# Kernel tuning notes

Measured on AMD Instinct MI355X. Metric: run time of the kernel, lower is better.

## Reference

```python
import jax, jax.numpy as jnp
import numpy as np

B, N, D, H = 2, 2048, 1024, 16
DH = D // H  # 64


def setup_inputs() -> dict:
    key = jax.random.key(0)
    k1, k2, k3, k4, k5 = jax.random.split(key, 5)
    x = jax.random.normal(k1, (B, N, D), dtype=jnp.float32)
    # per-head kqv Linear weights, stacked: [H, D, 3*DH] (acts as x @ W)
    W_kqv = jax.random.normal(k2, (H, D, 3 * DH), dtype=jnp.float32) * 0.02
    b_kqv = jax.random.normal(k3, (H, 3 * DH), dtype=jnp.float32) * 0.02
    W_proj = jax.random.normal(k4, (D, D), dtype=jnp.float32) * 0.02
    b_proj = jax.random.normal(k5, (D,), dtype=jnp.float32) * 0.02
    return {"x": x, "W_kqv": W_kqv, "b_kqv": b_kqv, "W_proj": W_proj, "b_proj": b_proj}


def reference(x, W_kqv, b_kqv, W_proj, b_proj):
    # per-head projections, all heads batched: [B, H, N, 3*DH]
    kqv = jnp.einsum('bnd,hde->bhne', x, W_kqv) + b_kqv[None, :, None, :]
    # original chunk order is k, q, v
    k, q, v = jnp.split(kqv, 3, axis=-1)  # each [B, H, N, DH]
    # scores: A = q @ k^T / sqrt(DH)  -> [B, H, N, N]
    A = jnp.einsum('bhnd,bhmd->bhnm', q, k) / jnp.sqrt(jnp.asarray(DH, x.dtype))
    causal = jnp.tril(jnp.ones((N, N), dtype=bool))
    A = jnp.where(causal[None, None, :, :], A, -jnp.inf)
    attn = jax.nn.softmax(A, axis=-1)
    sa = jnp.einsum('bhnm,bhmd->bhnd', attn, v)          # [B, H, N, DH]
    sa = sa.transpose(0, 2, 1, 3).reshape(B, N, D)        # concat heads
    out = sa @ W_proj.T + b_proj                          # output projection
    return out
```

## Files before the change

kernel.cpp:

```cpp
#include <hip/hip_runtime.h>
#include <hip/hip_bf16.h>
#include <cstdint>
#include <cstddef>

#define B_  2
#define N_  2048
#define D_  1024
#define H_  16
#define DH_ 64
#define E3_ 192

typedef __attribute__((ext_vector_type(8))) short short8;
typedef __attribute__((ext_vector_type(8))) unsigned short ushort8v;
typedef __attribute__((ext_vector_type(4))) float floatx4;

static __device__ __forceinline__ unsigned short f2bf(float f) {
  union { float f; unsigned u; } c; c.f = f;
  unsigned r = c.u + 0x7fffu + ((c.u >> 16) & 1u);
  return (unsigned short)(r >> 16);
}

#define MFMA(a,b,c) __builtin_amdgcn_mfma_f32_16x16x32_bf16((a),(b),(c),0,0,0)

#define GL_LDS16(g, l) __builtin_amdgcn_global_load_lds( \
    (const __attribute__((address_space(1))) void*)(g),  \
    (__attribute__((address_space(3))) void*)(l), 16, 0, 0)

__global__ __launch_bounds__(256) void k_prep(const float* __restrict__ x,
                                              const float* __restrict__ Wkqv,
                                              const float* __restrict__ Wproj,
                                              unsigned short* __restrict__ Xb,
                                              unsigned short* __restrict__ Wt,
                                              unsigned short* __restrict__ Wpb) {
  __shared__ float tile[64][65];
  int bx = blockIdx.x, t = threadIdx.x;
  if (bx < 2048 || bx >= 2816) {
    const float* in = (bx < 2048) ? x : Wproj;
    unsigned short* out = (bx < 2048) ? Xb : Wpb;
    int i = ((bx < 2048) ? bx : bx - 2816) * 256 + t;
    const float4* p = (const float4*)in + (size_t)i * 2;
    float4 a = p[0], b = p[1];
    ushort8v o;
    o[0]=f2bf(a.x); o[1]=f2bf(a.y); o[2]=f2bf(a.z); o[3]=f2bf(a.w);
    o[4]=f2bf(b.x); o[5]=f2bf(b.y); o[6]=f2bf(b.z); o[7]=f2bf(b.w);
    *((ushort8v*)out + i) = o;
    return;
  }
  int idx = bx - 2048;
  int d0 = (idx & 15) * 64, rem = idx >> 4;
  int cat = rem % 3, h = rem / 3, e0 = cat * 64;
  const float* Wp = Wkqv + (size_t)h * D_ * E3_;
  int dr = t >> 2, ec = (t & 3) * 16;
#pragma unroll
  for (int j = 0; j < 16; j += 4) {
    float4 wv = *(const float4*)&Wp[(size_t)(d0 + dr) * E3_ + e0 + ec + j];
    tile[dr][ec + j + 0] = wv.x; tile[dr][ec + j + 1] = wv.y;
    tile[dr][ec + j + 2] = wv.z; tile[dr][ec + j + 3] = wv.w;
  }
  __syncthreads();
  int er = t >> 2, dc = (t & 3) * 16;
  ushort8v o0, o1;
#pragma unroll
  for (int j = 0; j < 8; j++) o0[j] = f2bf(tile[dc + j][er]);
#pragma unroll
  for (int j = 0; j < 8; j++) o1[j] = f2bf(tile[dc + 8 + j][er]);
  size_t o = ((size_t)(cat * 1024 + h * 64 + er)) * D_ + d0 + dc;
  *(ushort8v*)&Wt[o]     = o0;
  *(ushort8v*)&Wt[o + 8] = o1;
}

__global__ __launch_bounds__(256) void k_qkv(const unsigned short* __restrict__ Xb,
                                             const unsigned short* __restrict__ Wt,
                                             const float* __restrict__ bkqv,
                                             unsigned short* __restrict__ Qb,
                                             unsigned short* __restrict__ Kb,
                                             unsigned short* __restrict__ Vt) {
  __shared__ unsigned short Alds[2][128 * 32];
  __shared__ unsigned short Blds[2][128 * 32];
  int t = threadIdx.x;
  int m0 = blockIdx.x * 128, c0 = blockIdx.y * 128;
  int wave = t >> 6, lane = t & 63, quad = lane >> 4, l16 = lane & 15;
  int wm = (wave >> 1) * 64, wn = (wave & 1) * 64;
  floatx4 acc[4][4];
#pragma unroll
  for (int i = 0; i < 4; i++)
#pragma unroll
    for (int j = 0; j < 4; j++) acc[i][j] = (floatx4){0.f, 0.f, 0.f, 0.f};

  const unsigned short* gA = Xb + (size_t)(m0 + wave * 32 + (lane >> 2)) * D_ + (lane & 3) * 8;
  const unsigned short* gB = Wt + (size_t)(c0 + wave * 32 + (lane >> 2)) * D_ + (lane & 3) * 8;
  int lofs = (wave * 32) * 32;

  GL_LDS16(gA,            &Alds[0][lofs]);
  GL_LDS16(gA + 16 * D_,  &Alds[0][lofs + 16 * 32]);
  GL_LDS16(gB,            &Blds[0][lofs]);
  GL_LDS16(gB + 16 * D_,  &Blds[0][lofs + 16 * 32]);

  for (int i = 0; i < 32; i++) {
    int buf = i & 1;
    __syncthreads();
    if (i + 1 < 32) {
      int k0 = (i + 1) * 32;
      GL_LDS16(gA + k0,            &Alds[buf ^ 1][lofs]);
      GL_LDS16(gA + k0 + 16 * D_,  &Alds[buf ^ 1][lofs + 16 * 32]);
      GL_LDS16(gB + k0,            &Blds[buf ^ 1][lofs]);
      GL_LDS16(gB + k0 + 16 * D_,  &Blds[buf ^ 1][lofs + 16 * 32]);
    }
    short8 a[4], b[4];
#pragma unroll
    for (int mi = 0; mi < 4; mi++) a[mi] = *(const short8*)&Alds[buf][(wm + mi * 16 + l16) * 32 + quad * 8];
#pragma unroll
    for (int ni = 0; ni < 4; ni++) b[ni] = *(const short8*)&Blds[buf][(wn + ni * 16 + l16) * 32 + quad * 8];
#pragma unroll
    for (int mi = 0; mi < 4; mi++)
#pragma unroll
      for (int ni = 0; ni < 4; ni++) acc[mi][ni] = MFMA(a[mi], b[ni], acc[mi][ni]);
  }

  int cat = c0 >> 10;
#pragma unroll
  for (int mi = 0; mi < 4; mi++)
#pragma unroll
    for (int ni = 0; ni < 4; ni++) {
      int colp = c0 + wn + ni * 16 + l16;
      int h = (colp >> 6) & 15;
      int e = colp & 63;
      int grow = m0 + wm + mi * 16 + quad * 4;
      int b = grow >> 11, n0 = grow & (N_ - 1);
      int bh = b * H_ + h;
      float bias = bkqv[h * E3_ + cat * 64 + e];
      floatx4 v = acc[mi][ni];
      if (cat == 0) {
        size_t base = ((size_t)bh * N_ + n0) * DH_ + e;
#pragma unroll
        for (int r = 0; r < 4; r++) Kb[base + (size_t)r * DH_] = f2bf(v[r] + bias);
      } else if (cat == 1) {
        size_t base = ((size_t)bh * N_ + n0) * DH_ + e;
#pragma unroll
        for (int r = 0; r < 4; r++) Qb[base + (size_t)r * DH_] = f2bf((v[r] + bias) * 0.125f);
      } else {
        ushort4 pk;
        pk.x = f2bf(v[0] + bias); pk.y = f2bf(v[1] + bias);
        pk.z = f2bf(v[2] + bias); pk.w = f2bf(v[3] + bias);
        *(ushort4*)&Vt[((size_t)bh * DH_ + e) * N_ + n0] = pk;
      }
    }
}

#define PSTR 72
__global__ __launch_bounds__(256) void k_flash(const unsigned short* __restrict__ Qb,
                                               const unsigned short* __restrict__ Kb,
                                               const unsigned short* __restrict__ Vt,
                                               unsigned short* __restrict__ sab) {
  int bh = blockIdx.x;
  int yr = blockIdx.y, g = yr >> 3, o = yr & 7;
  int qb = (g == 0) ? o : (g == 1) ? 31 - o : (g == 2) ? 8 + o : 23 - o;
  int q0b = qb * 64;
  int wave = threadIdx.x >> 6;
  int lane = threadIdx.x & 63, quad = lane >> 4, l16 = lane & 15;
  const unsigned short* Qp = Qb + (size_t)bh * N_ * DH_;
  const unsigned short* Kp = Kb + (size_t)bh * N_ * DH_;
  const unsigned short* Vp = Vt + (size_t)bh * DH_ * N_;
  __shared__ unsigned short Klds[2][2 * 64 * 32];
  __shared__ unsigned short Vlds[2][2 * 64 * 32];
  __shared__ unsigned short Plds[4][16 * PSTR];
  unsigned short* P = Plds[wave];

  int q0w = q0b + wave * 16;
  short8 qf0 = *(const short8*)&Qp[(q0w + l16) * DH_ + quad * 8];
  short8 qf1 = *(const short8*)&Qp[(q0w + l16) * DH_ + 32 + quad * 8];

  const unsigned short* gK = Kp + (size_t)(wave * 16 + (lane >> 2)) * DH_ + (lane & 3) * 8;
  const unsigned short* gV = Vp + (size_t)(wave * 16 + (lane >> 2)) * N_ + (lane & 3) * 8;
  int lofs = (wave * 16) * 32;

  floatx4 O[4];
  float lr[4];
#pragma unroll
  for (int r = 0; r < 4; r++) { O[r] = (floatx4){0.f, 0.f, 0.f, 0.f}; lr[r] = 0.f; }

  int nt = (q0b >> 6) + 1;
  GL_LDS16(gK,      &Klds[0][lofs]);
  GL_LDS16(gK + 32, &Klds[0][lofs + 64 * 32]);
  GL_LDS16(gV,      &Vlds[0][lofs]);
  GL_LDS16(gV + 32, &Vlds[0][lofs + 64 * 32]);

  for (int i = 0; i < nt; i++) {
    int buf = i & 1;
    __syncthreads();
    if (i + 1 < nt) {
      int kvn = (i + 1) << 6;
      GL_LDS16(gK + (size_t)kvn * DH_,      &Klds[buf ^ 1][lofs]);
      GL_LDS16(gK + (size_t)kvn * DH_ + 32, &Klds[buf ^ 1][lofs + 64 * 32]);
      GL_LDS16(gV + kvn,                    &Vlds[buf ^ 1][lofs]);
      GL_LDS16(gV + kvn + 32,               &Vlds[buf ^ 1][lofs + 64 * 32]);
    }
    short8 kf[4][2], vf[4][2];
#pragma unroll
    for (int c = 0; c < 4; c++) {
      kf[c][0] = *(const short8*)&Klds[buf][(c * 16 + l16) * 32 + quad * 8];
      kf[c][1] = *(const short8*)&Klds[buf][(64 + c * 16 + l16) * 32 + quad * 8];
      vf[c][0] = *(const short8*)&Vlds[buf][(c * 16 + l16) * 32 + quad * 8];
      vf[c][1] = *(const short8*)&Vlds[buf][(64 + c * 16 + l16) * 32 + quad * 8];
    }
    floatx4 s[4];
#pragma unroll
    for (int c = 0; c < 4; c++) {
      s[c] = (floatx4){0.f, 0.f, 0.f, 0.f};
      s[c] = MFMA(qf0, kf[c][0], s[c]);
      s[c] = MFMA(qf1, kf[c][1], s[c]);
    }
    if (i == nt - 1) {
#pragma unroll
      for (int c = 0; c < 4; c++)
#pragma unroll
        for (int r = 0; r < 4; r++) {
          int row = wave * 16 + quad * 4 + r;
          if (c * 16 + l16 > row) s[c][r] = -1e30f;
        }
    }
#pragma unroll
    for (int c = 0; c < 4; c++)
#pragma unroll
      for (int r = 0; r < 4; r++)
        s[c][r] = __builtin_amdgcn_exp2f(s[c][r] * 1.44269504f);
#pragma unroll
    for (int r = 0; r < 4; r++)
      lr[r] += (s[0][r] + s[1][r]) + (s[2][r] + s[3][r]);
#pragma unroll
    for (int c = 0; c < 4; c++)
#pragma unroll
      for (int r = 0; r < 4; r++)
        P[(quad * 4 + r) * PSTR + c * 16 + l16] = f2bf(s[c][r]);
    __asm__ volatile("s_waitcnt lgkmcnt(0)" ::: "memory");
    short8 pa0 = *(const short8*)&P[l16 * PSTR + quad * 8];
    short8 pa1 = *(const short8*)&P[l16 * PSTR + 32 + quad * 8];
    __asm__ volatile("" ::: "memory");
#pragma unroll
    for (int dt = 0; dt < 4; dt++) {
      O[dt] = MFMA(pa0, vf[dt][0], O[dt]);
      O[dt] = MFMA(pa1, vf[dt][1], O[dt]);
    }
  }
#pragma unroll
  for (int m = 1; m < 16; m <<= 1)
#pragma unroll
    for (int r = 0; r < 4; r++) lr[r] += __shfl_xor(lr[r], m);

  int b = bh >> 4, h = bh & 15;
#pragma unroll
  for (int r = 0; r < 4; r++) {
    float inv = 1.0f / lr[r];
    size_t base = ((size_t)b * N_ + q0w + quad * 4 + r) * D_ + h * DH_;
#pragma unroll
    for (int dt = 0; dt < 4; dt++) sab[base + dt * 16 + l16] = f2bf(O[dt][r] * inv);
  }
}

__global__ __launch_bounds__(256) void k_proj(const unsigned short* __restrict__ sab,
                                              const unsigned short* __restrict__ Wpb,
                                              const float* __restrict__ bproj,
                                              float* __restrict__ out) {
  __shared__ unsigned short Alds[2][2][64 * 32];
  __shared__ unsigned short Blds[2][2][64 * 32];
  int t = threadIdx.x;
  int m0 = blockIdx.x * 64, c0 = blockIdx.y * 64;
  int wave = t >> 6, lane = t & 63, quad = lane >> 4, l16 = lane & 15;
  int wm = (wave >> 1) * 32, wn = (wave & 1) * 32;
  floatx4 acc[2][2];
#pragma unroll
  for (int i = 0; i < 2; i++) { acc[i][0] = (floatx4){0,0,0,0}; acc[i][1] = (floatx4){0,0,0,0}; }

  const unsigned short* gA = sab + (size_t)(m0 + wave * 16 + (lane >> 2)) * D_ + (lane & 3) * 8;
  const unsigned short* gB = Wpb + (size_t)(c0 + wave * 16 + (lane >> 2)) * D_ + (lane & 3) * 8;
  int lofs = (wave * 16) * 32;

  GL_LDS16(gA,      &Alds[0][0][lofs]);
  GL_LDS16(gA + 32, &Alds[0][1][lofs]);
  GL_LDS16(gB,      &Blds[0][0][lofs]);
  GL_LDS16(gB + 32, &Blds[0][1][lofs]);

  for (int i = 0; i < 16; i++) {
    int buf = i & 1;
    __syncthreads();
    if (i + 1 < 16) {
      int k0 = (i + 1) * 64;
      GL_LDS16(gA + k0,      &Alds[buf ^ 1][0][lofs]);
      GL_LDS16(gA + k0 + 32, &Alds[buf ^ 1][1][lofs]);
      GL_LDS16(gB + k0,      &Blds[buf ^ 1][0][lofs]);
      GL_LDS16(gB + k0 + 32, &Blds[buf ^ 1][1][lofs]);
    }
#pragma unroll
    for (int kk = 0; kk < 2; kk++) {
      short8 a[2], b[2];
#pragma unroll
      for (int mi = 0; mi < 2; mi++) a[mi] = *(const short8*)&Alds[buf][kk][(wm + mi * 16 + l16) * 32 + quad * 8];
#pragma unroll
      for (int ni = 0; ni < 2; ni++) b[ni] = *(const short8*)&Blds[buf][kk][(wn + ni * 16 + l16) * 32 + quad * 8];
#pragma unroll
      for (int mi = 0; mi < 2; mi++)
#pragma unroll
        for (int ni = 0; ni < 2; ni++) acc[mi][ni] = MFMA(a[mi], b[ni], acc[mi][ni]);
    }
  }
#pragma unroll
  for (int mi = 0; mi < 2; mi++)
#pragma unroll
    for (int ni = 0; ni < 2; ni++) {
      int col = c0 + wn + ni * 16 + l16;
      int grow = m0 + wm + mi * 16 + quad * 4;
      float bias = bproj[col];
#pragma unroll
      for (int r = 0; r < 4; r++)
        out[(size_t)(grow + r) * D_ + col] = acc[mi][ni][r] + bias;
    }
}

extern "C" void kernel_launch(void* const* d_in, const int* in_sizes, int n_in,
                              void* d_out, int out_size, void* d_ws, size_t ws_size,
                              hipStream_t stream) {
  const float* x     = (const float*)d_in[0];
  const float* Wkqv  = (const float*)d_in[1];
  const float* bkqv  = (const float*)d_in[2];
  const float* Wproj = (const float*)d_in[3];
  const float* bproj = (const float*)d_in[4];
  float* out = (float*)d_out;

  char* w = (char*)d_ws;
  unsigned short* Xb  = (unsigned short*)(w);
  unsigned short* Wt  = (unsigned short*)(w + (8u  << 20));
  unsigned short* Wpb = (unsigned short*)(w + (14u << 20));
  unsigned short* Qb  = (unsigned short*)(w + (16u << 20));
  unsigned short* Kb  = (unsigned short*)(w + (24u << 20));
  unsigned short* Vt  = (unsigned short*)(w + (32u << 20));
  unsigned short* sa  = (unsigned short*)(w + (40u << 20));

  k_prep<<<2048 + 768 + 512, 256, 0, stream>>>(x, Wkqv, Wproj, Xb, Wt, Wpb);
  k_qkv<<<dim3(B_ * N_ / 128, 3072 / 128), 256, 0, stream>>>(Xb, Wt, bkqv, Qb, Kb, Vt);
  k_flash<<<dim3(B_ * H_, N_ / 64), 256, 0, stream>>>(Qb, Kb, Vt, sa);
  k_proj<<<dim3(B_ * N_ / 64, D_ / 64), 256, 0, stream>>>(sa, Wpb, bproj, out);
}
```

Baseline: 186.5 us.

## XOR-swizzle LDS tiles and stage QKV epilogue through LDS for coalesced stores

Applies an XOR swizzle to the global-to-LDS tile loads and the matching fragment reads in all three kernels, and swizzles the per-wave P buffer in the flash kernel without padding. This is meant to remove LDS bank conflicts on the 16-byte fragment reads. The QKV GEMM epilogue now writes bf16 results into reused LDS scratch and then issues 16-byte coalesced global stores for K, Q and transposed V, replacing scattered 2-byte and 8-byte stores. It adds an extra barrier and an LDS round trip in the epilogue, and the swizzle index maths must stay consistent between writers and readers.

Result: no change. 186.0 us (-0.2%).

```diff
diff --git a/kernel.cpp b/kernel.cpp
--- a/kernel.cpp
+++ b/kernel.cpp
@@ -87,9 +87,11 @@
 #pragma unroll
     for (int j = 0; j < 4; j++) acc[i][j] = (floatx4){0.f, 0.f, 0.f, 0.f};
 
-  const unsigned short* gA = Xb + (size_t)(m0 + wave * 32 + (lane >> 2)) * D_ + (lane & 3) * 8;
-  const unsigned short* gB = Wt + (size_t)(c0 + wave * 32 + (lane >> 2)) * D_ + (lane & 3) * 8;
+  int swz = ((lane & 3) ^ ((lane >> 3) & 3)) * 8;
+  const unsigned short* gA = Xb + (size_t)(m0 + wave * 32 + (lane >> 2)) * D_ + swz;
+  const unsigned short* gB = Wt + (size_t)(c0 + wave * 32 + (lane >> 2)) * D_ + swz;
   int lofs = (wave * 32) * 32;
+  int xr = ((l16 >> 1) & 3) * 8;
 
   GL_LDS16(gA,            &Alds[0][lofs]);
   GL_LDS16(gA + 16 * D_,  &Alds[0][lofs + 16 * 32]);
@@ -108,46 +110,65 @@
     }
     short8 a[4], b[4];
 #pragma unroll
-    for (int mi = 0; mi < 4; mi++) a[mi] = *(const short8*)&Alds[buf][(wm + mi * 16 + l16) * 32 + quad * 8];
-#pragma unroll
-    for (int ni = 0; ni < 4; ni++) b[ni] = *(const short8*)&Blds[buf][(wn + ni * 16 + l16) * 32 + quad * 8];
+    for (int mi = 0; mi < 4; mi++) a[mi] = *(const short8*)&Alds[buf][(wm + mi * 16 + l16) * 32 + ((quad * 8) ^ xr)];
+#pragma unroll
+    for (int ni = 0; ni < 4; ni++) b[ni] = *(const short8*)&Blds[buf][(wn + ni * 16 + l16) * 32 + ((quad * 8) ^ xr)];
 #pragma unroll
     for (int mi = 0; mi < 4; mi++)
 #pragma unroll
       for (int ni = 0; ni < 4; ni++) acc[mi][ni] = MFMA(a[mi], b[ni], acc[mi][ni]);
   }
 
+  __syncthreads();
+  unsigned short* scratch = ((wave < 2) ? &Alds[0][0] : &Blds[0][0]) + (wave & 1) * 4096;
   int cat = c0 >> 10;
+  float scale = (cat == 1) ? 0.125f : 1.0f;
 #pragma unroll
   for (int mi = 0; mi < 4; mi++)
 #pragma unroll
     for (int ni = 0; ni < 4; ni++) {
-      int colp = c0 + wn + ni * 16 + l16;
-      int h = (colp >> 6) & 15;
-      int e = colp & 63;
-      int grow = m0 + wm + mi * 16 + quad * 4;
+      int lc = ni * 16 + l16;
+      int colp = c0 + wn + lc;
+      int h = (colp >> 6) & 15, e = colp & 63;
+      float bias = bkqv[h * E3_ + cat * 64 + e];
+#pragma unroll
+      for (int r = 0; r < 4; r++) {
+        unsigned short val = f2bf((acc[mi][ni][r] + bias) * scale);
+        int lr = mi * 16 + quad * 4 + r;
+        if (cat < 2)
+          scratch[lr * 64 + (((lc >> 3) ^ (lr & 7)) * 8) + (lc & 7)] = val;
+        else
+          scratch[lc * 64 + (((lr >> 3) ^ (lc & 7)) * 8) + (lr & 7)] = val;
+      }
+    }
+  __asm__ volatile("s_waitcnt lgkmcnt(0)" ::: "memory");
+  int l8 = lane & 7, lh = lane >> 3;
+  if (cat < 2) {
+    unsigned short* dst = (cat == 0) ? Kb : Qb;
+#pragma unroll
+    for (int j = 0; j < 8; j++) {
+      int lr = j * 8 + lh;
+      short8 vv = *(const short8*)&scratch[lr * 64 + ((l8 ^ lh) * 8)];
+      int grow = m0 + wm + lr;
       int b = grow >> 11, n0 = grow & (N_ - 1);
-      int bh = b * H_ + h;
-      float bias = bkqv[h * E3_ + cat * 64 + e];
-      floatx4 v = acc[mi][ni];
-      if (cat == 0) {
-        size_t base = ((size_t)bh * N_ + n0) * DH_ + e;
-#pragma unroll
-        for (int r = 0; r < 4; r++) Kb[base + (size_t)r * DH_] = f2bf(v[r] + bias);
-      } else if (cat == 1) {
-        size_t base = ((size_t)bh * N_ + n0) * DH_ + e;
-#pragma unroll
-        for (int r = 0; r < 4; r++) Qb[base + (size_t)r * DH_] = f2bf((v[r] + bias) * 0.125f);
-      } else {
-        ushort4 pk;
-        pk.x = f2bf(v[0] + bias); pk.y = f2bf(v[1] + bias);
-        pk.z = f2bf(v[2] + bias); pk.w = f2bf(v[3] + bias);
-        *(ushort4*)&Vt[((size_t)bh * DH_ + e) * N_ + n0] = pk;
-      }
-    }
-}
-
-#define PSTR 72
+      int colp = c0 + wn + l8 * 8;
+      int h = (colp >> 6) & 15, e0 = colp & 63;
+      *(short8*)&dst[((size_t)(b * H_ + h) * N_ + n0) * DH_ + e0] = vv;
+    }
+  } else {
+#pragma unroll
+    for (int j = 0; j < 8; j++) {
+      int le = j * 8 + lh;
+      short8 vv = *(const short8*)&scratch[le * 64 + ((l8 ^ lh) * 8)];
+      int colp = c0 + wn + le;
+      int h = (colp >> 6) & 15, e = colp & 63;
+      int grow = m0 + wm;
+      int b = grow >> 11, n0 = (grow & (N_ - 1)) + l8 * 8;
+      *(short8*)&Vt[((size_t)(b * H_ + h) * DH_ + e) * N_ + n0] = vv;
+    }
+  }
+}
+
 __global__ __launch_bounds__(256) void k_flash(const unsigned short* __restrict__ Qb,
                                                const unsigned short* __restrict__ Kb,
                                                const unsigned short* __restrict__ Vt,
@@ -163,16 +184,19 @@
   const unsigned short* Vp = Vt + (size_t)bh * DH_ * N_;
   __shared__ unsigned short Klds[2][2 * 64 * 32];
   __shared__ unsigned short Vlds[2][2 * 64 * 32];
-  __shared__ unsigned short Plds[4][16 * PSTR];
+  __shared__ unsigned short Plds[4][16 * 64];
   unsigned short* P = Plds[wave];
 
   int q0w = q0b + wave * 16;
   short8 qf0 = *(const short8*)&Qp[(q0w + l16) * DH_ + quad * 8];
   short8 qf1 = *(const short8*)&Qp[(q0w + l16) * DH_ + 32 + quad * 8];
 
-  const unsigned short* gK = Kp + (size_t)(wave * 16 + (lane >> 2)) * DH_ + (lane & 3) * 8;
-  const unsigned short* gV = Vp + (size_t)(wave * 16 + (lane >> 2)) * N_ + (lane & 3) * 8;
+  int swz = ((lane & 3) ^ ((lane >> 3) & 3)) * 8;
+  const unsigned short* gK = Kp + (size_t)(wave * 16 + (lane >> 2)) * DH_ + swz;
+  const unsigned short* gV = Vp + (size_t)(wave * 16 + (lane >> 2)) * N_ + swz;
   int lofs = (wave * 16) * 32;
+  int xr = ((l16 >> 1) & 3) * 8;
+  int pxr = l16 & 7;
 
   floatx4 O[4];
   float lr[4];
@@ -198,10 +222,10 @@
     short8 kf[4][2], vf[4][2];
 #pragma unroll
     for (int c = 0; c < 4; c++) {
-      kf[c][0] = *(const short8*)&Klds[buf][(c * 16 + l16) * 32 + quad * 8];
-      kf[c][1] = *(const short8*)&Klds[buf][(64 + c * 16 + l16) * 32 + quad * 8];
-      vf[c][0] = *(const short8*)&Vlds[buf][(c * 16 + l16) * 32 + quad * 8];
-      vf[c][1] = *(const short8*)&Vlds[buf][(64 + c * 16 + l16) * 32 + quad * 8];
+      kf[c][0] = *(const short8*)&Klds[buf][(c * 16 + l16) * 32 + ((quad * 8) ^ xr)];
+      kf[c][1] = *(const short8*)&Klds[buf][(64 + c * 16 + l16) * 32 + ((quad * 8) ^ xr)];
+      vf[c][0] = *(const short8*)&Vlds[buf][(c * 16 + l16) * 32 + ((quad * 8) ^ xr)];
+      vf[c][1] = *(const short8*)&Vlds[buf][(64 + c * 16 + l16) * 32 + ((quad * 8) ^ xr)];
     }
     floatx4 s[4];
 #pragma unroll
@@ -228,13 +252,17 @@
     for (int r = 0; r < 4; r++)
       lr[r] += (s[0][r] + s[1][r]) + (s[2][r] + s[3][r]);
 #pragma unroll
-    for (int c = 0; c < 4; c++)
-#pragma unroll
-      for (int r = 0; r < 4; r++)
-        P[(quad * 4 + r) * PSTR + c * 16 + l16] = f2bf(s[c][r]);
+    for (int c = 0; c < 4; c++) {
+      int ch = c * 2 + (l16 >> 3);
+#pragma unroll
+      for (int r = 0; r < 4; r++) {
+        int row = quad * 4 + r;
+        P[row * 64 + ((ch ^ (row & 7)) * 8) + (l16 & 7)] = f2bf(s[c][r]);
+      }
+    }
     __asm__ volatile("s_waitcnt lgkmcnt(0)" ::: "memory");
-    short8 pa0 = *(const short8*)&P[l16 * PSTR + quad * 8];
-    short8 pa1 = *(const short8*)&P[l16 * PSTR + 32 + quad * 8];
+    short8 pa0 = *(const short8*)&P[l16 * 64 + ((quad ^ pxr) * 8)];
+    short8 pa1 = *(const short8*)&P[l16 * 64 + (((quad + 4) ^ pxr) * 8)];
     __asm__ volatile("" ::: "memory");
 #pragma unroll
     for (int dt = 0; dt < 4; dt++) {
@@ -271,9 +299,11 @@
 #pragma unroll
   for (int i = 0; i < 2; i++) { acc[i][0] = (floatx4){0,0,0,0}; acc[i][1] = (floatx4){0,0,0,0}; }
 
-  const unsigned short* gA = sab + (size_t)(m0 + wave * 16 + (lane >> 2)) * D_ + (lane & 3) * 8;
-  const unsigned short* gB = Wpb + (size_t)(c0 + wave * 16 + (lane >> 2)) * D_ + (lane & 3) * 8;
+  int swz = ((lane & 3) ^ ((lane >> 3) & 3)) * 8;
+  const unsigned short* gA = sab + (size_t)(m0 + wave * 16 + (lane >> 2)) * D_ + swz;
+  const unsigned short* gB = Wpb + (size_t)(c0 + wave * 16 + (lane >> 2)) * D_ + swz;
   int lofs = (wave * 16) * 32;
+  int xr = ((l16 >> 1) & 3) * 8;
 
   GL_LDS16(gA,      &Alds[0][0][lofs]);
   GL_LDS16(gA + 32, &Alds[0][1][lofs]);
@@ -294,9 +324,9 @@
     for (int kk = 0; kk < 2; kk++) {
       short8 a[2], b[2];
 #pragma unroll
-      for (int mi = 0; mi < 2; mi++) a[mi] = *(const short8*)&Alds[buf][kk][(wm + mi * 16 + l16) * 32 + quad * 8];
-#pragma unroll
-      for (int ni = 0; ni < 2; ni++) b[ni] = *(const short8*)&Blds[buf][kk][(wn + ni * 16 + l16) * 32 + quad * 8];
+      for (int mi = 0; mi < 2; mi++) a[mi] = *(const short8*)&Alds[buf][kk][(wm + mi * 16 + l16) * 32 + ((quad * 8) ^ xr)];
+#pragma unroll
+      for (int ni = 0; ni < 2; ni++) b[ni] = *(const short8*)&Blds[buf][kk][(wn + ni * 16 + l16) * 32 + ((quad * 8) ^ xr)];
 #pragma unroll
       for (int mi = 0; mi < 2; mi++)
 #pragma unroll
```
